# Kernel optimization log

Measured on AMD Instinct MI355X. Metric: run time of the kernel, lower is better.

## Reference

```python
import jax, jax.numpy as jnp
import numpy as np
import math

B, H, N, D = 8, 8, 4096, 64
M = 64          # select_number (CUR rank)
N_ITER = 6      # Newton-Schulz iterations in iterative_inv


def setup_inputs() -> dict:
    key = jax.random.key(0)
    k1, k2, k3 = jax.random.split(key, 3)
    Q = jax.random.normal(k1, (B, H, N, D), jnp.float32)
    K = jax.random.normal(k2, (B, H, N, D), jnp.float32)
    V = jax.random.normal(k3, (B, H, N, D), jnp.float32)
    mask = jnp.ones((B, N), dtype=bool)
    return {"Q": Q, "K": K, "V": V, "mask": mask}


def _top_k_sum_select(T, mask, m):
    # select_type='sum', absolute=False -> score = row sum over D
    somme = T.sum(-1)                                    # [B,H,N]
    somme = jnp.where(mask[:, None, :], somme, -jnp.finfo(somme.dtype).max)
    idx = jnp.argsort(-somme, axis=-1)[..., :m]          # descending top-m, [B,H,M]
    nt = jnp.take_along_axis(T, idx[..., None], axis=2)  # [B,H,M,D]
    return nt, idx


def _iterative_inv(mat, n_iter=N_ITER):
    # init_option='original': global-max scaled transpose
    m = mat.shape[-1]
    I = jnp.eye(m, dtype=mat.dtype)
    Km = mat
    Vm = Km.swapaxes(-1, -2) / jnp.max(Km.sum(-2))
    for _ in range(n_iter):
        KV = Km @ Vm
        Vm = 0.25 * Vm @ (13.0 * I - KV @ (15.0 * I - KV @ (7.0 * I - KV)))
    return Vm


def reference(Q, K, V, mask):
    Qs = Q / math.sqrt(D)
    nc, _ = _top_k_sum_select(K, mask, M)        # column landmarks of K
    nr, r_idx = _top_k_sum_select(Qs, mask, M)   # row landmarks of Q
    c = jnp.einsum('bhnd,bhmd->bhnm', Qs, nc)    # [B,H,N,M]
    r = jnp.einsum('bhmd,bhnd->bhmn', nr, K)     # [B,H,M,N]
    r = jnp.where(mask[:, None, None, :], r, -jnp.finfo(r.dtype).max)
    kernel_1 = jax.nn.softmax(c, axis=-1)        # [B,H,N,M]
    # m_matrix_composition: gather rows of kernel_1 at r_idx -> [B,H,M,M]
    u = jnp.take_along_axis(kernel_1, r_idx[..., None], axis=2)
    kernel_3 = jax.nn.softmax(r, axis=-1)        # [B,H,M,N]
    kernel_2_inv = _iterative_inv(u)             # [B,H,M,M]
    RV = kernel_3 @ V                            # [B,H,M,D]
    X = kernel_1 @ (kernel_2_inv @ RV)           # [B,H,N,D]
    return X
```

## Files before the change

### kernel.cpp

```cpp
#include <hip/hip_runtime.h>
#include <math.h>

#define NSEQ 4096
#define NCH  8

#define OFF_SUMK 0u
#define OFF_SUMQ 262144u
#define OFF_WTH  0u
#define OFF_WTL  131072u
#define OFF_U    262144u
#define OFF_NC   524288u
#define OFF_NR   786432u
#define OFF_VM   1048576u
#define OFF_NCH  1310720u
#define OFF_NCL  1441792u
#define OFF_PMAX 1572864u
#define OFF_PSUM 1638400u
#define OFF_HMAX 1703936u
#define OFF_PRV  1704000u

typedef unsigned short u16;
typedef short short8 __attribute__((ext_vector_type(8)));
typedef short bf4 __attribute__((ext_vector_type(4)));
typedef float f32x4 __attribute__((ext_vector_type(4)));

__device__ __forceinline__ u16 f2bf(float x) {
    unsigned u = __float_as_uint(x);
    unsigned r = (u + 0x7FFFu + ((u >> 16) & 1u)) >> 16;
    return (u16)r;
}
__device__ __forceinline__ void splitbf(float x, u16& h, u16& l) {
    unsigned u = __float_as_uint(x);
    h = (u16)(u >> 16);
    float hf = __uint_as_float(u & 0xFFFF0000u);
    l = f2bf(x - hf);
}

__device__ __forceinline__ short8 ldfrag(const u16* base, int row, int k0) {
    int byte = (row << 7) + (k0 << 1);
    byte ^= (row & 7) << 4;
    return *(const short8*)((const char*)base + byte);
}
__device__ __forceinline__ void st4(u16* base, int row, int c0, ushort4 v) {
    int byte = (row << 7) + (c0 << 1);
    byte ^= (row & 7) << 4;
    *(ushort4*)((char*)base + byte) = v;
}
__device__ __forceinline__ void stb16(u16* base, int row, int c, u16 v) {
    int byte = (row << 7) + (c << 1);
    byte ^= (row & 7) << 4;
    *(u16*)((char*)base + byte) = v;
}
__device__ __forceinline__ unsigned vt_byte(int d, int n) {
    unsigned byte = ((unsigned)d << 7) + ((unsigned)n << 1);
    byte ^= (unsigned)(d & 15) << 3;
    return byte;
}

__device__ __forceinline__ f32x4 MFMA(short8 a, short8 b, f32x4 c) {
    return __builtin_amdgcn_mfma_f32_16x16x32_bf16(a, b, c, 0, 0, 0);
}

__device__ __forceinline__ void stage64(const float* __restrict__ g, u16* Lh, u16* Ll,
                                        int t, float scale) {
#pragma unroll
    for (int i = 0; i < 4; i++) {
        int e = t + 256 * i;
        int row = e >> 4, c0 = (e & 15) << 2;
        float4 v = *(const float4*)(g + row * 64 + c0);
        float vv[4] = {v.x * scale, v.y * scale, v.z * scale, v.w * scale};
        ushort4 h, l;
        splitbf(vv[0], h.x, l.x); splitbf(vv[1], h.y, l.y);
        splitbf(vv[2], h.z, l.z); splitbf(vv[3], h.w, l.w);
        st4(Lh, row, c0, h); st4(Ll, row, c0, l);
    }
}

__device__ __forceinline__ void copy64bf(u16* dst, const u16* __restrict__ src, int t) {
#pragma unroll
    for (int i = 0; i < 4; i++) {
        int e = t + 256 * i;
        int row = e >> 4, c0 = (e & 15) << 2;
        ushort4 v = *(const ushort4*)(src + row * 64 + c0);
        st4(dst, row, c0, v);
    }
}

__device__ __forceinline__ void loadT64(float* dst, const float* __restrict__ src, int t) {
    for (int e = t; e < 1024; e += 256) {
        int m = e >> 4, k0 = (e & 15) << 2;
        float4 v = *(const float4*)(src + m * 64 + k0);
        dst[(k0 + 0) * 64 + m] = v.x;
        dst[(k0 + 1) * 64 + m] = v.y;
        dst[(k0 + 2) * 64 + m] = v.z;
        dst[(k0 + 3) * 64 + m] = v.w;
    }
}
__device__ __forceinline__ void mm64add(const float* Acm, const float* Brm,
                                        float acc[4][4], int i0, int j0) {
#pragma unroll 8
    for (int k = 0; k < 64; k++) {
        float4 a = *(const float4*)(Acm + k * 64 + i0);
        float4 b = *(const float4*)(Brm + k * 64 + j0);
        acc[0][0] += a.x * b.x; acc[0][1] += a.x * b.y; acc[0][2] += a.x * b.z; acc[0][3] += a.x * b.w;
        acc[1][0] += a.y * b.x; acc[1][1] += a.y * b.y; acc[1][2] += a.y * b.z; acc[1][3] += a.y * b.w;
        acc[2][0] += a.z * b.x; acc[2][1] += a.z * b.y; acc[2][2] += a.z * b.z; acc[2][3] += a.z * b.w;
        acc[3][0] += a.w * b.x; acc[3][1] += a.w * b.y; acc[3][2] += a.w * b.z; acc[3][3] += a.w * b.w;
    }
}
__device__ __forceinline__ void mm64(const float* Acm, const float* Brm,
                                     float acc[4][4], int i0, int j0) {
#pragma unroll
    for (int r = 0; r < 4; r++)
#pragma unroll
        for (int c = 0; c < 4; c++) acc[r][c] = 0.f;
    mm64add(Acm, Brm, acc, i0, j0);
}
__device__ __forceinline__ void writeN64(float* dst, const float acc[4][4], int i0, int j0, float s) {
#pragma unroll
    for (int r = 0; r < 4; r++) {
        float4 v;
        v.x = s * acc[r][0]; v.y = s * acc[r][1]; v.z = s * acc[r][2]; v.w = s * acc[r][3];
        *(float4*)(dst + (i0 + r) * 64 + j0) = v;
    }
}

__global__ __launch_bounds__(256) void k_sums(const float* __restrict__ Qg,
                                              const float* __restrict__ Kg, float* ws) {
    int t = threadIdx.x;
    size_t base4 = (size_t)blockIdx.x * 1024;
    float qs[4], ks[4];
#pragma unroll
    for (int i = 0; i < 4; i++) {
        int e = t + 256 * i;
        float4 v = *(const float4*)(Qg + (base4 + e) * 4);
        qs[i] = (v.x + v.y) + (v.z + v.w);
        float4 w = *(const float4*)(Kg + (base4 + e) * 4);
        ks[i] = (w.x + w.y) + (w.z + w.w);
    }
#pragma unroll
    for (int i = 0; i < 4; i++) {
#pragma unroll
        for (int s = 1; s < 16; s <<= 1) {
            qs[i] += __shfl_xor(qs[i], s);
            ks[i] += __shfl_xor(ks[i], s);
        }
    }
    if ((t & 15) == 0) {
        size_t row = (size_t)blockIdx.x * 64 + (t >> 4);
#pragma unroll
        for (int i = 0; i < 4; i++) {
            ws[OFF_SUMQ + row + 16 * i] = qs[i];
            ws[OFF_SUMK + row + 16 * i] = ks[i];
        }
    }
}

__global__ __launch_bounds__(256) void k_select(const float* __restrict__ Qg,
                                                const float* __restrict__ Kg, float* ws) {
    int head = blockIdx.x, sel = blockIdx.y, t = threadIdx.x;
    __shared__ int hist[257];
    __shared__ int idx_s[64];
    __shared__ unsigned s_prefix;
    __shared__ int s_need, s_cnt, s_win;
    __shared__ int wred[4];
    const float* scores = ws + (sel ? OFF_SUMQ : OFF_SUMK) + (size_t)head * 4096;
    unsigned uu[16];
#pragma unroll
    for (int i = 0; i < 16; i++) {
        unsigned u = __float_as_uint(scores[t + 256 * i]);
        uu[i] = (u & 0x80000000u) ? ~u : (u | 0x80000000u);
    }
    if (t == 0) { s_prefix = 0u; s_need = 64; }
    __syncthreads();
#pragma unroll
    for (int p = 0; p < 4; p++) {
        hist[t] = 0;
        if (t == 0) hist[256] = 0;
        __syncthreads();
        unsigned pref = s_prefix;
        int sh = 32 - 8 * p;
        int dsh = 24 - 8 * p;
#pragma unroll
        for (int i = 0; i < 16; i++) {
            bool active = (p == 0) || ((uu[i] >> sh) == (pref >> sh));
            if (active) atomicAdd(&hist[(uu[i] >> dsh) & 255], 1);
        }
        __syncthreads();
        for (int s = 1; s < 256; s <<= 1) {
            int v = (t + s < 256) ? hist[t + s] : 0;
            __syncthreads();
            hist[t] += v;
            __syncthreads();
        }
        int need = s_need;
        __syncthreads();
        if (hist[t] >= need && (t == 255 || hist[t + 1] < need)) {
            s_need = need - ((t == 255) ? 0 : hist[t + 1]);
            s_prefix = pref | ((unsigned)t << dsh);
        }
        __syncthreads();
    }
    unsigned thr = s_prefix;
    int needEq = s_need;
    if (t == 0) s_cnt = 0;
    __syncthreads();
    unsigned eqm = 0;
#pragma unroll
    for (int i = 0; i < 16; i++) {
        if (uu[i] > thr) { int pos = atomicAdd(&s_cnt, 1); idx_s[pos] = t + 256 * i; }
        else if (uu[i] == thr) eqm |= (1u << i);
    }
    __syncthreads();
    int base = 64 - needEq;
    int lane = t & 63, wid = t >> 6;
    for (int r = 0; r < needEq; r++) {
        int mymin = 0x7FFFFFFF;
#pragma unroll
        for (int i = 0; i < 16; i++)
            if ((eqm >> i) & 1) mymin = min(mymin, t + 256 * i);
#pragma unroll
        for (int s = 1; s < 64; s <<= 1) mymin = min(mymin, __shfl_xor(mymin, s));
        if (lane == 0) wred[wid] = mymin;
        __syncthreads();
        if (t == 0) {
            int wv = min(min(wred[0], wred[1]), min(wred[2], wred[3]));
            s_win = wv;
            idx_s[base + r] = wv;
        }
        __syncthreads();
        int wv = s_win;
        if ((wv & 255) == t) eqm &= ~(1u << (wv >> 8));
        __syncthreads();
    }
    const float* src = sel ? Qg : Kg;
    float* dst = ws + (sel ? OFF_NR : OFF_NC) + (size_t)head * 4096;
    u16* dh = (u16*)(ws + OFF_NCH) + (size_t)head * 4096;
    u16* dl = (u16*)(ws + OFF_NCL) + (size_t)head * 4096;
    float scl = sel ? 0.125f : 1.0f;
    for (int e = t; e < 4096; e += 256) {
        int m = e >> 6, d = e & 63;
        float v = src[((size_t)head * NSEQ + (size_t)idx_s[m]) * 64 + d] * scl;
        dst[e] = v;
        if (!sel) { u16 h, l; splitbf(v, h, l); dh[e] = h; dl[e] = l; }
    }
}

__global__ __launch_bounds__(256) void k_u(float* ws) {
    int head = blockIdx.x, t = threadIdx.x;
    __shared__ __align__(16) float A_s[4096];
    __shared__ __align__(16) float B_s[4096];
    __shared__ float colpart[1024];
    loadT64(A_s, ws + OFF_NR + (size_t)head * 4096, t);
    loadT64(B_s, ws + OFF_NC + (size_t)head * 4096, t);
    __syncthreads();
    int ti = t >> 4, tj = t & 15, i0 = ti << 2, j0 = tj << 2;
    float acc[4][4];
    mm64(A_s, B_s, acc, i0, j0);
#pragma unroll
    for (int r = 0; r < 4; r++) {
        float m0 = fmaxf(fmaxf(acc[r][0], acc[r][1]), fmaxf(acc[r][2], acc[r][3]));
        m0 = fmaxf(m0, __shfl_xor(m0, 1)); m0 = fmaxf(m0, __shfl_xor(m0, 2));
        m0 = fmaxf(m0, __shfl_xor(m0, 4)); m0 = fmaxf(m0, __shfl_xor(m0, 8));
        float s = 0.f;
#pragma unroll
        for (int c = 0; c < 4; c++) { acc[r][c] = __expf(acc[r][c] - m0); s += acc[r][c]; }
        s += __shfl_xor(s, 1); s += __shfl_xor(s, 2);
        s += __shfl_xor(s, 4); s += __shfl_xor(s, 8);
#pragma unroll
        for (int c = 0; c < 4; c++) acc[r][c] = acc[r][c] / s;
    }
    float* u = ws + OFF_U + (size_t)head * 4096;
#pragma unroll
    for (int r = 0; r < 4; r++) {
        float4 v; v.x = acc[r][0]; v.y = acc[r][1]; v.z = acc[r][2]; v.w = acc[r][3];
        *(float4*)(u + (i0 + r) * 64 + j0) = v;
    }
#pragma unroll
    for (int c = 0; c < 4; c++)
        colpart[ti * 64 + j0 + c] = acc[0][c] + acc[1][c] + acc[2][c] + acc[3][c];
    __syncthreads();
    if (t < 64) {
        float cs = 0.f;
#pragma unroll
        for (int g = 0; g < 16; g++) cs += colpart[g * 64 + t];
        float v = cs;
#pragma unroll
        for (int s = 1; s < 64; s <<= 1) v = fmaxf(v, __shfl_xor(v, s));
        if (t == 0) ws[OFF_HMAX + head] = v;
    }
}

__global__ __launch_bounds__(256) void k_nsinv(float* ws) {
    int head = blockIdx.x, t = threadIdx.x;
    __shared__ __align__(16) u16 KmH[4096], KmL[4096];
    __shared__ __align__(16) u16 VmNH[4096], VmNL[4096];
    __shared__ __align__(16) u16 VmTH[4096], VmTL[4096];
    __shared__ __align__(16) u16 KVH[4096], KVL[4096];
    __shared__ __align__(16) u16 BtH[4096], BtL[4096];
    __shared__ __align__(16) float Vmf[4096];

    int w = t >> 6, lane = t & 63, lrow = lane & 15, lk = (lane >> 4) << 3;
    int mrow0 = 16 * w + ((lane >> 4) << 2);

    float g = ws[OFF_HMAX + lane];
#pragma unroll
    for (int s = 1; s < 64; s <<= 1) g = fmaxf(g, __shfl_xor(g, s));
    float ginv = 1.0f / g;

    const float* u = ws + OFF_U + (size_t)head * 4096;
#pragma unroll
    for (int i = 0; i < 4; i++) {
        int e = t + 256 * i;
        int row = e >> 4, c0 = (e & 15) << 2;
        float4 v = *(const float4*)(u + row * 64 + c0);
        float vv[4] = {v.x, v.y, v.z, v.w};
        ushort4 h4, l4;
        splitbf(vv[0], h4.x, l4.x); splitbf(vv[1], h4.y, l4.y);
        splitbf(vv[2], h4.z, l4.z); splitbf(vv[3], h4.w, l4.w);
        st4(KmH, row, c0, h4); st4(KmL, row, c0, l4);
        float sv[4] = {vv[0] * ginv, vv[1] * ginv, vv[2] * ginv, vv[3] * ginv};
        splitbf(sv[0], h4.x, l4.x); splitbf(sv[1], h4.y, l4.y);
        splitbf(sv[2], h4.z, l4.z); splitbf(sv[3], h4.w, l4.w);
        st4(VmTH, row, c0, h4); st4(VmTL, row, c0, l4);
#pragma unroll
        for (int k = 0; k < 4; k++) {
            u16 h, l; splitbf(sv[k], h, l);
            stb16(VmNH, c0 + k, row, h); stb16(VmNL, c0 + k, row, l);
            Vmf[(c0 + k) * 64 + row] = sv[k];
        }
    }
    __syncthreads();

    f32x4 cv[4];
    for (int it = 0; it < 6; it++) {
        {
            short8 a0h = ldfrag(KmH, 16 * w + lrow, lk);
            short8 a0l = ldfrag(KmL, 16 * w + lrow, lk);
            short8 a1h = ldfrag(KmH, 16 * w + lrow, 32 + lk);
            short8 a1l = ldfrag(KmL, 16 * w + lrow, 32 + lk);
#pragma unroll
            for (int nt = 0; nt < 4; nt++) {
                f32x4 acc = (f32x4){0.f, 0.f, 0.f, 0.f};
                short8 bh = ldfrag(VmTH, 16 * nt + lrow, lk);
                short8 bl = ldfrag(VmTL, 16 * nt + lrow, lk);
                acc = MFMA(a0h, bh, acc); acc = MFMA(a0l, bh, acc); acc = MFMA(a0h, bl, acc);
                bh = ldfrag(VmTH, 16 * nt + lrow, 32 + lk);
                bl = ldfrag(VmTL, 16 * nt + lrow, 32 + lk);
                acc = MFMA(a1h, bh, acc); acc = MFMA(a1l, bh, acc); acc = MFMA(a1h, bl, acc);
                cv[nt] = acc;
            }
        }
#pragma unroll
        for (int nt = 0; nt < 4; nt++)
#pragma unroll
            for (int j = 0; j < 4; j++) {
                int m = mrow0 + j, n = 16 * nt + lrow;
                float v = cv[nt][j];
                u16 h, l; splitbf(v, h, l);
                stb16(KVH, m, n, h); stb16(KVL, m, n, l);
                float b = ((m == n) ? 7.f : 0.f) - v;
                splitbf(b, h, l);
                stb16(BtH, n, m, h); stb16(BtL, n, m, l);
            }
        __syncthreads();
        {
            short8 a0h = ldfrag(KVH, 16 * w + lrow, lk);
            short8 a0l = ldfrag(KVL, 16 * w + lrow, lk);
            short8 a1h = ldfrag(KVH, 16 * w + lrow, 32 + lk);
            short8 a1l = ldfrag(KVL, 16 * w + lrow, 32 + lk);
#pragma unroll
            for (int nt = 0; nt < 4; nt++) {
                f32x4 acc = (f32x4){0.f, 0.f, 0.f, 0.f};
                short8 bh = ldfrag(BtH, 16 * nt + lrow, lk);
                short8 bl = ldfrag(BtL, 16 * nt + lrow, lk);
                acc = MFMA(a0h, bh, acc); acc = MFMA(a0l, bh, acc); acc = MFMA(a0h, bl, acc);
                bh = ldfrag(BtH, 16 * nt + lrow, 32 + lk);
                bl = ldfrag(BtL, 16 * nt + lrow, 32 + lk);
                acc = MFMA(a1h, bh, acc); acc = MFMA(a1l, bh, acc); acc = MFMA(a1h, bl, acc);
                cv[nt] = acc;
            }
        }
        __syncthreads();
#pragma unroll
        for (int nt = 0; nt < 4; nt++)
#pragma unroll
            for (int j = 0; j < 4; j++) {
                int m = mrow0 + j, n = 16 * nt + lrow;
                float b = ((m == n) ? 15.f : 0.f) - cv[nt][j];
                u16 h, l; splitbf(b, h, l);
                stb16(BtH, n, m, h); stb16(BtL, n, m, l);
            }
        __syncthreads();
        {
            short8 a0h = ldfrag(KVH, 16 * w + lrow, lk);
            short8 a0l = ldfrag(KVL, 16 * w + lrow, lk);
            short8 a1h = ldfrag(KVH, 16 * w + lrow, 32 + lk);
            short8 a1l = ldfrag(KVL, 16 * w + lrow, 32 + lk);
#pragma unroll
            for (int nt = 0; nt < 4; nt++) {
                f32x4 acc = (f32x4){0.f, 0.f, 0.f, 0.f};
                short8 bh = ldfrag(BtH, 16 * nt + lrow, lk);
                short8 bl = ldfrag(BtL, 16 * nt + lrow, lk);
                acc = MFMA(a0h, bh, acc); acc = MFMA(a0l, bh, acc); acc = MFMA(a0h, bl, acc);
                bh = ldfrag(BtH, 16 * nt + lrow, 32 + lk);
                bl = ldfrag(BtL, 16 * nt + lrow, 32 + lk);
                acc = MFMA(a1h, bh, acc); acc = MFMA(a1l, bh, acc); acc = MFMA(a1h, bl, acc);
                cv[nt] = acc;
            }
        }
        __syncthreads();
#pragma unroll
        for (int nt = 0; nt < 4; nt++)
#pragma unroll
            for (int j = 0; j < 4; j++) {
                int m = mrow0 + j, n = 16 * nt + lrow;
                float b = ((m == n) ? 13.f : 0.f) - cv[nt][j];
                u16 h, l; splitbf(b, h, l);
                stb16(BtH, n, m, h); stb16(BtL, n, m, l);
            }
        __syncthreads();
        {
            short8 a0h = ldfrag(VmNH, 16 * w + lrow, lk);
            short8 a0l = ldfrag(VmNL, 16 * w + lrow, lk);
            short8 a1h = ldfrag(VmNH, 16 * w + lrow, 32 + lk);
            short8 a1l = ldfrag(VmNL, 16 * w + lrow, 32 + lk);
#pragma unroll
            for (int nt = 0; nt < 4; nt++) {
                f32x4 acc = (f32x4){0.f, 0.f, 0.f, 0.f};
                short8 bh = ldfrag(BtH, 16 * nt + lrow, lk);
                short8 bl = ldfrag(BtL, 16 * nt + lrow, lk);
                acc = MFMA(a0h, bh, acc); acc = MFMA(a0l, bh, acc); acc = MFMA(a0h, bl, acc);
                bh = ldfrag(BtH, 16 * nt + lrow, 32 + lk);
                bl = ldfrag(BtL, 16 * nt + lrow, 32 + lk);
                acc = MFMA(a1h, bh, acc); acc = MFMA(a1l, bh, acc); acc = MFMA(a1h, bl, acc);
                cv[nt] = acc;
            }
        }
        __syncthreads();
#pragma unroll
        for (int nt = 0; nt < 4; nt++)
#pragma unroll
            for (int j = 0; j < 4; j++) {
                int m = mrow0 + j, n = 16 * nt + lrow;
                float v = 0.25f * cv[nt][j];
                u16 h, l; splitbf(v, h, l);
                stb16(VmNH, m, n, h); stb16(VmNL, m, n, l);
                stb16(VmTH, n, m, h); stb16(VmTL, n, m, l);
                Vmf[m * 64 + n] = v;
            }
        __syncthreads();
    }

    float* vm = ws + OFF_VM + (size_t)head * 4096;
#pragma unroll
    for (int i = 0; i < 4; i++) {
        int e = t + 256 * i;
        int row = e >> 4, c0 = (e & 15) << 2;
        *(float4*)(vm + row * 64 + c0) = *(const float4*)(Vmf + row * 64 + c0);
    }
}

__global__ __launch_bounds__(256) void k_rvp(const float* __restrict__ Kg,
                                             const float* __restrict__ Vg, float* ws) {
    int head = blockIdx.x, ch = blockIdx.y, t = threadIdx.x;
    const int nsub = (NSEQ / 64) / NCH;
    __shared__ __align__(16) u16 Kh[4096], Kl[4096];
    __shared__ __align__(16) u16 Vth[4096], Vtl[4096];
    int w = t >> 6, lane = t & 63, lrow = lane & 15, g = lane >> 4;
    int lk = g << 3;
    int mrow0 = 16 * w + (g << 2);
    int krow = t >> 4, kc0 = (t & 15) << 2;
    int vn0 = (t & 15) << 2, vd0 = (t >> 4) << 2;

    short8 nh0, nl0, nh1, nl1;
    {
        const float* nr = ws + OFF_NR + (size_t)head * 4096 + (size_t)(16 * w + lrow) * 64;
        float a[8], b[8];
        *(float4*)(a + 0) = *(const float4*)(nr + lk);
        *(float4*)(a + 4) = *(const float4*)(nr + lk + 4);
        *(float4*)(b + 0) = *(const float4*)(nr + 32 + lk);
        *(float4*)(b + 4) = *(const float4*)(nr + 32 + lk + 4);
#pragma unroll
        for (int i = 0; i < 8; i++) {
            u16 h, l;
            splitbf(a[i], h, l); nh0[i] = (short)h; nl0[i] = (short)l;
            splitbf(b[i], h, l); nh1[i] = (short)h; nl1[i] = (short)l;
        }
    }

    f32x4 rv[4];
#pragma unroll
    for (int dt = 0; dt < 4; dt++) rv[dt] = (f32x4){0.f, 0.f, 0.f, 0.f};
    float mrow = -INFINITY, srow = 0.f;

    const int rows = NSEQ / NCH;
    const float* Kb = Kg + ((size_t)head * NSEQ + (size_t)ch * rows) * 64;
    const float* Vb = Vg + ((size_t)head * NSEQ + (size_t)ch * rows) * 64;

    float4 kreg[4], vreg[4];
#pragma unroll
    for (int i = 0; i < 4; i++)
        kreg[i] = *(const float4*)(Kb + (krow + 16 * i) * 64 + kc0);
#pragma unroll
    for (int k = 0; k < 4; k++)
        vreg[k] = *(const float4*)(Vb + (vn0 + k) * 64 + vd0);

    for (int s8 = 0; s8 < nsub; s8++) {
#pragma unroll
        for (int i = 0; i < 4; i++) {
            ushort4 h4, l4;
            splitbf(kreg[i].x, h4.x, l4.x); splitbf(kreg[i].y, h4.y, l4.y);
            splitbf(kreg[i].z, h4.z, l4.z); splitbf(kreg[i].w, h4.w, l4.w);
            st4(Kh, krow + 16 * i, kc0, h4); st4(Kl, krow + 16 * i, kc0, l4);
        }
#pragma unroll
        for (int dd = 0; dd < 4; dd++) {
            float x0 = ((const float*)&vreg[0])[dd];
            float x1 = ((const float*)&vreg[1])[dd];
            float x2 = ((const float*)&vreg[2])[dd];
            float x3 = ((const float*)&vreg[3])[dd];
            ushort4 h4, l4;
            splitbf(x0, h4.x, l4.x); splitbf(x1, h4.y, l4.y);
            splitbf(x2, h4.z, l4.z); splitbf(x3, h4.w, l4.w);
            unsigned byte = vt_byte(vd0 + dd, vn0);
            *(ushort4*)((char*)Vth + byte) = h4;
            *(ushort4*)((char*)Vtl + byte) = l4;
        }
        __syncthreads();
        if (s8 + 1 < nsub) {
            const float* Kn = Kb + (s8 + 1) * 4096;
            const float* Vn = Vb + (s8 + 1) * 4096;
#pragma unroll
            for (int i = 0; i < 4; i++)
                kreg[i] = *(const float4*)(Kn + (krow + 16 * i) * 64 + kc0);
#pragma unroll
            for (int k = 0; k < 4; k++)
                vreg[k] = *(const float4*)(Vn + (vn0 + k) * 64 + vd0);
        }

        f32x4 cv[4];
#pragma unroll
        for (int nt = 0; nt < 4; nt++) {
            f32x4 acc = (f32x4){0.f, 0.f, 0.f, 0.f};
            short8 ah = ldfrag(Kh, 16 * nt + lrow, lk);
            short8 al = ldfrag(Kl, 16 * nt + lrow, lk);
            acc = MFMA(ah, nh0, acc); acc = MFMA(al, nh0, acc); acc = MFMA(ah, nl0, acc);
            ah = ldfrag(Kh, 16 * nt + lrow, 32 + lk);
            al = ldfrag(Kl, 16 * nt + lrow, 32 + lk);
            acc = MFMA(ah, nh1, acc); acc = MFMA(al, nh1, acc); acc = MFMA(ah, nl1, acc);
            cv[nt] = acc;
        }
        float m0 = cv[0][0];
#pragma unroll
        for (int nt = 0; nt < 4; nt++)
#pragma unroll
            for (int j = 0; j < 4; j++) m0 = fmaxf(m0, cv[nt][j]);
        m0 = fmaxf(m0, __shfl_xor(m0, 16));
        m0 = fmaxf(m0, __shfl_xor(m0, 32));
        float mnew = fmaxf(mrow, m0);
        float sc = __expf(mrow - mnew);
        float ps = 0.f;
#pragma unroll
        for (int nt = 0; nt < 4; nt++)
#pragma unroll
            for (int j = 0; j < 4; j++) {
                float p = __expf(cv[nt][j] - mnew);
                cv[nt][j] = p; ps += p;
            }
        ps += __shfl_xor(ps, 16);
        ps += __shfl_xor(ps, 32);
        srow = srow * sc + ps;
        mrow = mnew;
        float scl[4];
#pragma unroll
        for (int j = 0; j < 4; j++) scl[j] = __shfl(sc, (g << 2) + j);
#pragma unroll
        for (int dt = 0; dt < 4; dt++)
#pragma unroll
            for (int j = 0; j < 4; j++) rv[dt][j] *= scl[j];
        short8 pah[2], pal[2];
#pragma unroll
        for (int h2 = 0; h2 < 2; h2++)
#pragma unroll
            for (int i = 0; i < 8; i++) {
                u16 hh, ll;
                splitbf(cv[2 * h2 + (i >> 2)][i & 3], hh, ll);
                pah[h2][i] = (short)hh; pal[h2][i] = (short)ll;
            }
#pragma unroll
        for (int dt = 0; dt < 4; dt++) {
            int drow = 16 * dt + lrow;
#pragma unroll
            for (int h2 = 0; h2 < 2; h2++) {
                bf4 xh0 = *(const bf4*)((const char*)Vth + vt_byte(drow, 32 * h2 + 4 * g));
                bf4 xh1 = *(const bf4*)((const char*)Vth + vt_byte(drow, 32 * h2 + 16 + 4 * g));
                bf4 xl0 = *(const bf4*)((const char*)Vtl + vt_byte(drow, 32 * h2 + 4 * g));
                bf4 xl1 = *(const bf4*)((const char*)Vtl + vt_byte(drow, 32 * h2 + 16 + 4 * g));
                short8 bh = __builtin_shufflevector(xh0, xh1, 0, 1, 2, 3, 4, 5, 6, 7);
                short8 bl = __builtin_shufflevector(xl0, xl1, 0, 1, 2, 3, 4, 5, 6, 7);
                rv[dt] = MFMA(pah[h2], bh, rv[dt]);
                rv[dt] = MFMA(pal[h2], bh, rv[dt]);
                rv[dt] = MFMA(pah[h2], bl, rv[dt]);
            }
        }
        __syncthreads();
    }
    size_t pb = (size_t)(head * NCH + ch) * 64;
    if (lane < 16) {
        ws[OFF_PMAX + pb + 16 * w + lane] = mrow;
        ws[OFF_PSUM + pb + 16 * w + lane] = srow;
    }
#pragma unroll
    for (int dt = 0; dt < 4; dt++)
#pragma unroll
        for (int j = 0; j < 4; j++)
            ws[OFF_PRV + (pb + mrow0 + j) * 64 + 16 * dt + lrow] = rv[dt][j];
}

__global__ __launch_bounds__(256) void k_comb(float* ws) {
    int head = blockIdx.x, t = threadIdx.x;
    const int nch = NCH;
    __shared__ __align__(16) float A_s[4096];
    __shared__ __align__(16) float B_s[4096];
    loadT64(A_s, ws + OFF_VM + (size_t)head * 4096, t);
    int ti = t >> 4, tj = t & 15, i0 = ti << 2, j0 = tj << 2;
    const float* pm = ws + OFF_PMAX + (size_t)head * nch * 64;
    const float* psv = ws + OFF_PSUM + (size_t)head * nch * 64;
    const float* prv = ws + OFF_PRV + (size_t)head * nch * 4096;
    float gm[4] = {-INFINITY, -INFINITY, -INFINITY, -INFINITY};
    for (int c8 = 0; c8 < nch; c8++)
#pragma unroll
        for (int r = 0; r < 4; r++) gm[r] = fmaxf(gm[r], pm[c8 * 64 + i0 + r]);
    float stot[4] = {0.f, 0.f, 0.f, 0.f};
    float racc[4][4];
#pragma unroll
    for (int r = 0; r < 4; r++)
#pragma unroll
        for (int c = 0; c < 4; c++) racc[r][c] = 0.f;
    for (int c8 = 0; c8 < nch; c8++) {
#pragma unroll
        for (int r = 0; r < 4; r++) {
            float w = __expf(pm[c8 * 64 + i0 + r] - gm[r]);
            stot[r] += w * psv[c8 * 64 + i0 + r];
            float4 v = *(const float4*)(prv + (size_t)(c8 * 64 + i0 + r) * 64 + j0);
            racc[r][0] += w * v.x; racc[r][1] += w * v.y;
            racc[r][2] += w * v.z; racc[r][3] += w * v.w;
        }
    }
#pragma unroll
    for (int r = 0; r < 4; r++)
#pragma unroll
        for (int c = 0; c < 4; c++) racc[r][c] /= stot[r];
    writeN64(B_s, racc, i0, j0, 1.f);
    __syncthreads();
    float acc[4][4];
    mm64(A_s, B_s, acc, i0, j0);
    u16* wth = (u16*)(ws + OFF_WTH) + (size_t)head * 4096;
    u16* wtl = (u16*)(ws + OFF_WTL) + (size_t)head * 4096;
#pragma unroll
    for (int r = 0; r < 4; r++)
#pragma unroll
        for (int c = 0; c < 4; c++) {
            u16 h, l; splitbf(acc[r][c], h, l);
            wth[(j0 + c) * 64 + (i0 + r)] = h;
            wtl[(j0 + c) * 64 + (i0 + r)] = l;
        }
}

__global__ __launch_bounds__(256) void k_final(const float* __restrict__ Qg, float* ws,
                                               float* __restrict__ out) {
    int tile = blockIdx.x, head = blockIdx.y, t = threadIdx.x;
    __shared__ __align__(16) u16 Ah[4096], Al[4096];
    __shared__ __align__(16) u16 Bh[4096], Bl[4096];
    __shared__ __align__(16) float C[64 * 68];
    const float* Qt = Qg + ((size_t)head * NSEQ + (size_t)tile * 64) * 64;
    stage64(Qt, Ah, Al, t, 0.125f);
    copy64bf(Bh, (const u16*)(ws + OFF_NCH) + (size_t)head * 4096, t);
    copy64bf(Bl, (const u16*)(ws + OFF_NCL) + (size_t)head * 4096, t);
    __syncthreads();
    int w = t >> 6, lane = t & 63, lrow = lane & 15, lk = (lane >> 4) << 3;
    int mrow0 = 16 * w + ((lane >> 4) << 2);
    short8 a0h = ldfrag(Ah, 16 * w + lrow, lk);
    short8 a0l = ldfrag(Al, 16 * w + lrow, lk);
    short8 a1h = ldfrag(Ah, 16 * w + lrow, 32 + lk);
    short8 a1l = ldfrag(Al, 16 * w + lrow, 32 + lk);
    f32x4 sa[4];
#pragma unroll
    for (int nt = 0; nt < 4; nt++) {
        f32x4 acc = (f32x4){0.f, 0.f, 0.f, 0.f};
        short8 bh = ldfrag(Bh, 16 * nt + lrow, lk);
        short8 bl = ldfrag(Bl, 16 * nt + lrow, lk);
        acc = MFMA(a0h, bh, acc); acc = MFMA(a0l, bh, acc); acc = MFMA(a0h, bl, acc);
        bh = ldfrag(Bh, 16 * nt + lrow, 32 + lk);
        bl = ldfrag(Bl, 16 * nt + lrow, 32 + lk);
        acc = MFMA(a1h, bh, acc); acc = MFMA(a1l, bh, acc); acc = MFMA(a1h, bl, acc);
        sa[nt] = acc;
    }
#pragma unroll
    for (int j = 0; j < 4; j++) {
        float m0 = fmaxf(fmaxf(sa[0][j], sa[1][j]), fmaxf(sa[2][j], sa[3][j]));
        m0 = fmaxf(m0, __shfl_xor(m0, 1)); m0 = fmaxf(m0, __shfl_xor(m0, 2));
        m0 = fmaxf(m0, __shfl_xor(m0, 4)); m0 = fmaxf(m0, __shfl_xor(m0, 8));
        float ps = 0.f;
#pragma unroll
        for (int nt = 0; nt < 4; nt++) {
            float p = __expf(sa[nt][j] - m0);
            sa[nt][j] = p; ps += p;
        }
        ps += __shfl_xor(ps, 1); ps += __shfl_xor(ps, 2);
        ps += __shfl_xor(ps, 4); ps += __shfl_xor(ps, 8);
        float inv = 1.f / ps;
#pragma unroll
        for (int nt = 0; nt < 4; nt++) sa[nt][j] *= inv;
    }
    __syncthreads();
#pragma unroll
    for (int nt = 0; nt < 4; nt++)
#pragma unroll
        for (int j = 0; j < 4; j++) {
            u16 h, l; splitbf(sa[nt][j], h, l);
            stb16(Ah, mrow0 + j, 16 * nt + lrow, h);
            stb16(Al, mrow0 + j, 16 * nt + lrow, l);
        }
    copy64bf(Bh, (const u16*)(ws + OFF_WTH) + (size_t)head * 4096, t);
    copy64bf(Bl, (const u16*)(ws + OFF_WTL) + (size_t)head * 4096, t);
    __syncthreads();
    short8 p0h = ldfrag(Ah, 16 * w + lrow, lk);
    short8 p0l = ldfrag(Al, 16 * w + lrow, lk);
    short8 p1h = ldfrag(Ah, 16 * w + lrow, 32 + lk);
    short8 p1l = ldfrag(Al, 16 * w + lrow, 32 + lk);
#pragma unroll
    for (int dt = 0; dt < 4; dt++) {
        f32x4 x = (f32x4){0.f, 0.f, 0.f, 0.f};
        short8 bh = ldfrag(Bh, 16 * dt + lrow, lk);
        short8 bl = ldfrag(Bl, 16 * dt + lrow, lk);
        x = MFMA(p0h, bh, x); x = MFMA(p0l, bh, x); x = MFMA(p0h, bl, x);
        bh = ldfrag(Bh, 16 * dt + lrow, 32 + lk);
        bl = ldfrag(Bl, 16 * dt + lrow, 32 + lk);
        x = MFMA(p1h, bh, x); x = MFMA(p1l, bh, x); x = MFMA(p1h, bl, x);
#pragma unroll
        for (int j = 0; j < 4; j++) C[(mrow0 + j) * 68 + 16 * dt + lrow] = x[j];
    }
    __syncthreads();
    float* op = out + ((size_t)head * NSEQ + (size_t)tile * 64) * 64;
#pragma unroll
    for (int i = 0; i < 4; i++) {
        int e = t + 256 * i;
        int row = e >> 4, c0 = (e & 15) << 2;
        *(float4*)(op + row * 64 + c0) = *(const float4*)(C + row * 68 + c0);
    }
}

extern "C" void kernel_launch(void* const* d_in, const int* in_sizes, int n_in,
                              void* d_out, int out_size, void* d_ws, size_t ws_size,
                              hipStream_t stream) {
    const float* Q = (const float*)d_in[0];
    const float* K = (const float*)d_in[1];
    const float* V = (const float*)d_in[2];
    float* ws = (float*)d_ws;
    float* out = (float*)d_out;

    k_sums<<<4096, 256, 0, stream>>>(Q, K, ws);
    k_select<<<dim3(64, 2), 256, 0, stream>>>(Q, K, ws);
    k_u<<<64, 256, 0, stream>>>(ws);
    k_rvp<<<dim3(64, NCH), 256, 0, stream>>>(K, V, ws);
    k_nsinv<<<64, 256, 0, stream>>>(ws);
    k_comb<<<64, 256, 0, stream>>>(ws);
    k_final<<<dim3(64, 64), 256, 0, stream>>>(Q, ws, out);
}
```

Before: 145.0 us.

## Fuse K row-sum computation into k_rvp to avoid a separate pass over K

Moves the K row-sum scoring out of k_sums and computes it inside k_rvp, which already streams K in registers. K-landmark selection now runs as a separate launch after k_rvp, and Q selection runs before it. This removes one full read of K (64 MB) from k_sums. In exchange there is an extra kernel launch, and the work is serialized so that K selection waits for the rvp pass. Correctness depends on k_rvp not using the K selection results, and on it covering every row in its subtiles.

Result: slower. 154.5 us (+6.6%).

```diff
diff --git a/kernel.cpp b/kernel.cpp
--- a/kernel.cpp
+++ b/kernel.cpp
@@ -125,40 +125,34 @@
     }
 }
 
-__global__ __launch_bounds__(256) void k_sums(const float* __restrict__ Qg,
-                                              const float* __restrict__ Kg, float* ws) {
+__global__ __launch_bounds__(256) void k_sums(const float* __restrict__ Qg, float* ws) {
     int t = threadIdx.x;
     size_t base4 = (size_t)blockIdx.x * 1024;
-    float qs[4], ks[4];
+    float qs[4];
 #pragma unroll
     for (int i = 0; i < 4; i++) {
         int e = t + 256 * i;
         float4 v = *(const float4*)(Qg + (base4 + e) * 4);
         qs[i] = (v.x + v.y) + (v.z + v.w);
-        float4 w = *(const float4*)(Kg + (base4 + e) * 4);
-        ks[i] = (w.x + w.y) + (w.z + w.w);
     }
 #pragma unroll
     for (int i = 0; i < 4; i++) {
 #pragma unroll
-        for (int s = 1; s < 16; s <<= 1) {
+        for (int s = 1; s < 16; s <<= 1)
             qs[i] += __shfl_xor(qs[i], s);
-            ks[i] += __shfl_xor(ks[i], s);
-        }
     }
     if ((t & 15) == 0) {
         size_t row = (size_t)blockIdx.x * 64 + (t >> 4);
 #pragma unroll
-        for (int i = 0; i < 4; i++) {
+        for (int i = 0; i < 4; i++)
             ws[OFF_SUMQ + row + 16 * i] = qs[i];
-            ws[OFF_SUMK + row + 16 * i] = ks[i];
-        }
     }
 }
 
 __global__ __launch_bounds__(256) void k_select(const float* __restrict__ Qg,
-                                                const float* __restrict__ Kg, float* ws) {
-    int head = blockIdx.x, sel = blockIdx.y, t = threadIdx.x;
+                                                const float* __restrict__ Kg, float* ws,
+                                                int sel) {
+    int head = blockIdx.x, t = threadIdx.x;
     __shared__ int hist[257];
     __shared__ int idx_s[64];
     __shared__ unsigned s_prefix;
@@ -507,6 +501,20 @@
         vreg[k] = *(const float4*)(Vb + (vn0 + k) * 64 + vd0);
 
     for (int s8 = 0; s8 < nsub; s8++) {
+        {
+            float rs[4];
+#pragma unroll
+            for (int i = 0; i < 4; i++) {
+                rs[i] = (kreg[i].x + kreg[i].y) + (kreg[i].z + kreg[i].w);
+#pragma unroll
+                for (int s = 1; s < 16; s <<= 1) rs[i] += __shfl_xor(rs[i], s);
+            }
+            if ((t & 15) == 0) {
+                size_t rb = (size_t)head * 4096 + (size_t)ch * rows + (size_t)s8 * 64 + krow;
+#pragma unroll
+                for (int i = 0; i < 4; i++) ws[OFF_SUMK + rb + 16 * i] = rs[i];
+            }
+        }
 #pragma unroll
         for (int i = 0; i < 4; i++) {
             ushort4 h4, l4;
@@ -761,10 +769,11 @@
     float* ws = (float*)d_ws;
     float* out = (float*)d_out;
 
-    k_sums<<<4096, 256, 0, stream>>>(Q, K, ws);
-    k_select<<<dim3(64, 2), 256, 0, stream>>>(Q, K, ws);
+    k_sums<<<4096, 256, 0, stream>>>(Q, ws);
+    k_select<<<64, 256, 0, stream>>>(Q, K, ws, 1);
+    k_rvp<<<dim3(64, NCH), 256, 0, stream>>>(K, V, ws);
+    k_select<<<64, 256, 0, stream>>>(Q, K, ws, 0);
     k_u<<<64, 256, 0, stream>>>(ws);
-    k_rvp<<<dim3(64, NCH), 256, 0, stream>>>(K, V, ws);
     k_nsinv<<<64, 256, 0, stream>>>(ws);
     k_comb<<<64, 256, 0, stream>>>(ws);
     k_final<<<dim3(64, 64), 256, 0, stream>>>(Q, ws, out);
```
